# Kernel optimization log

Hardware: AMD Instinct MI355X
Metric: run time of the kernel (lower is better)

## Reference

```python
import jax, jax.numpy as jnp
import numpy as np

NUM_HEADS = 16

def setup_inputs() -> dict:
    key = jax.random.key(0)
    k1, k2, k3 = jax.random.split(key, 3)
    B, N, C = 4, 1024, 1024
    x = jax.random.normal(k1, (B, N, C), dtype=jnp.float32)
    w_qkv = jax.random.normal(k2, (C, 3 * C), dtype=jnp.float32) * (C ** -0.5)
    b_qkv = jnp.zeros((3 * C,), dtype=jnp.float32)
    w_proj = jax.random.normal(k3, (C, C), dtype=jnp.float32) * (C ** -0.5)
    b_proj = jnp.zeros((C,), dtype=jnp.float32)
    return {"x": x, "w_qkv": w_qkv, "b_qkv": b_qkv, "w_proj": w_proj, "b_proj": b_proj}

def reference(x, w_qkv, b_qkv, w_proj, b_proj):
    B, N, C = x.shape
    H = NUM_HEADS
    D = C // H
    scale = D ** -0.5
    # qkv projection: [B,N,3C] -> [3,B,H,N,D]
    qkv = (x @ w_qkv + b_qkv).reshape(B, N, 3, H, D).transpose(2, 0, 3, 1, 4)
    q, k, v = qkv[0], qkv[1], qkv[2]
    q = q * scale
    attn = jnp.einsum('bhnd,bhmd->bhnm', q, k)  # full N x N scores
    attn = jax.nn.softmax(attn, axis=-1)
    out = jnp.einsum('bhnm,bhmd->bhnd', attn, v)  # [B,H,N,D]
    out = out.transpose(0, 2, 1, 3).reshape(B, N, C)
    return out @ w_proj + b_proj
```

## Files before the change

### kernel.cpp

```cpp
#include <hip/hip_runtime.h>

typedef unsigned short u16;
typedef unsigned int u32;
typedef __attribute__((ext_vector_type(8))) short bf16x8;
typedef __attribute__((ext_vector_type(4))) float f32x4;
typedef __attribute__((ext_vector_type(16))) float f32x16;

#define LOG2E 1.4426950408889634f
#define QSCALE (0.125f * LOG2E)

__device__ __forceinline__ u16 f2bf(float f) {
  union { float f; u32 u; } x; x.f = f;
  u32 r = x.u + 0x7fffu + ((x.u >> 16) & 1u);
  return (u16)(r >> 16);
}

__device__ __forceinline__ u32 cvtpk(float a, float b) {
  u32 r;
  asm("v_cvt_pk_bf16_f32 %0, %1, %2" : "=v"(r) : "v"(a), "v"(b));
  return r;
}

__device__ __forceinline__ bf16x8 mkfrag(u32 a, u32 b, u32 c, u32 d) {
  union { u32 w[4]; bf16x8 v; } u;
  u.w[0] = a; u.w[1] = b; u.w[2] = c; u.w[3] = d;
  return u.v;
}

__device__ __forceinline__ void gload_lds16(const void* g, void* l) {
  __builtin_amdgcn_global_load_lds((const __attribute__((address_space(1))) u32*)g,
                                   (__attribute__((address_space(3))) u32*)l, 16, 0, 0);
}

__global__ __launch_bounds__(256) void k_cvt_x(const float* __restrict__ in, u16* __restrict__ out) {
  int i = blockIdx.x * 256 + threadIdx.x;
  const float4* p = (const float4*)in;
  float4 a = p[i * 2], b = p[i * 2 + 1];
  uint4 o;
  o.x = (u32)f2bf(a.x) | ((u32)f2bf(a.y) << 16);
  o.y = (u32)f2bf(a.z) | ((u32)f2bf(a.w) << 16);
  o.z = (u32)f2bf(b.x) | ((u32)f2bf(b.y) << 16);
  o.w = (u32)f2bf(b.z) | ((u32)f2bf(b.w) << 16);
  ((uint4*)out)[i] = o;
}

__global__ __launch_bounds__(256) void k_transpose_cvt(const float* __restrict__ src, u16* __restrict__ dst,
                                                       int R, int Cc) {
  __shared__ float tile[32][33];
  int c0 = blockIdx.x * 32, r0 = blockIdx.y * 32;
  int tx = threadIdx.x, ty = threadIdx.y;
  #pragma unroll
  for (int j = 0; j < 4; ++j)
    tile[ty * 4 + j][tx] = src[(r0 + ty * 4 + j) * Cc + c0 + tx];
  __syncthreads();
  #pragma unroll
  for (int j = 0; j < 4; ++j) {
    int cl = ty * 4 + j;
    dst[(c0 + cl) * R + r0 + tx] = f2bf(tile[tx][cl]);
  }
}

template <int EPI, int NBN>
__global__ __launch_bounds__(256) void k_gemm(const u16* __restrict__ A, const u16* __restrict__ Bt,
                                              const float* __restrict__ bias,
                                              u16* __restrict__ oq, u16* __restrict__ ok,
                                              u16* __restrict__ ovt, float* __restrict__ of) {
  __shared__ u16 lds[24576];
  const int tid = threadIdx.x;
  const int l = tid & 63, w = tid >> 6;
  const int wm = w >> 1, wn = w & 1;
  const int lr = l & 15, lh = l >> 4;
  const int cpx = gridDim.x >> 3;
  const int wg = (blockIdx.x & 7) * cpx + (blockIdx.x >> 3);
  const int bn = wg % NBN, bm = wg / NBN;

  f32x4 acc[4][4] = {};
  const int e = tid * 8;
  const u16* gA = A + (bm * 128 + (e >> 5)) * 1024 + (e & 31);
  const u16* gB = Bt + (bn * 128 + (e >> 5)) * 1024 + (e & 31);

  #define GSTAGE(kk, b)                                              \
    do {                                                             \
      gload_lds16(gA + (kk),         lds + (b) * 8192 + e);          \
      gload_lds16(gA + (kk) + 65536, lds + (b) * 8192 + e + 2048);   \
      gload_lds16(gB + (kk),         lds + (b) * 8192 + 4096 + e);   \
      gload_lds16(gB + (kk) + 65536, lds + (b) * 8192 + 4096 + e + 2048); \
    } while (0)

  GSTAGE(0, 0);
  GSTAGE(32, 1);
  int cur = 0, nxt = 2;

  for (int it = 0; it < 32; ++it) {
    if (it < 31) asm volatile("s_waitcnt vmcnt(4)" ::: "memory");
    else         asm volatile("s_waitcnt vmcnt(0)" ::: "memory");
    __builtin_amdgcn_s_barrier();
    __builtin_amdgcn_sched_barrier(0);

    if (it < 30) GSTAGE((it + 2) * 32, nxt);

    const u16* Asc = lds + cur * 8192;
    const u16* Bsc = lds + cur * 8192 + 4096;
    bf16x8 af[4], bfr[4];
    #pragma unroll
    for (int mi = 0; mi < 4; ++mi)
      af[mi] = *(const bf16x8*)(Asc + (wm * 64 + mi * 16 + lr) * 32 + lh * 8);
    #pragma unroll
    for (int ni = 0; ni < 4; ++ni)
      bfr[ni] = *(const bf16x8*)(Bsc + (wn * 64 + ni * 16 + lr) * 32 + lh * 8);
    #pragma unroll
    for (int mi = 0; mi < 4; ++mi)
      #pragma unroll
      for (int ni = 0; ni < 4; ++ni)
        acc[mi][ni] = __builtin_amdgcn_mfma_f32_16x16x32_bf16(af[mi], bfr[ni], acc[mi][ni], 0, 0, 0);

    cur = (cur == 2) ? 0 : cur + 1;
    nxt = (nxt == 2) ? 0 : nxt + 1;
  }
  #undef GSTAGE

  if (EPI == 0) {
    #pragma unroll
    for (int ni = 0; ni < 4; ++ni) {
      int col = bn * 128 + wn * 64 + ni * 16 + lr;
      float bb = bias[col];
      #pragma unroll
      for (int mi = 0; mi < 4; ++mi) {
        int row = bm * 128 + wm * 64 + mi * 16 + lh * 4;
        #pragma unroll
        for (int r = 0; r < 4; ++r)
          of[(row + r) * (NBN * 128) + col] = acc[mi][ni][r] + bb;
      }
    }
  } else {
    const int s = bn >> 3;
    __syncthreads();
    if (s < 2) {
      u16* dst = (s == 0) ? oq : ok;
      const float sc = (s == 0) ? QSCALE : 1.0f;
      #pragma unroll
      for (int ni = 0; ni < 4; ++ni) {
        int cl = wn * 64 + ni * 16 + lr;
        float bb = bias[bn * 128 + cl];
        #pragma unroll
        for (int mi = 0; mi < 4; ++mi) {
          int rl = wm * 64 + mi * 16 + lh * 4;
          #pragma unroll
          for (int r = 0; r < 4; ++r)
            lds[(rl + r) * 136 + cl] = f2bf((acc[mi][ni][r] + bb) * sc);
        }
      }
      __syncthreads();
      const int row = tid >> 1, half = tid & 1;
      const int h0 = ((bn * 128) & 1023) >> 6;
      const int b = (bm * 128) >> 10, n0 = (bm * 128) & 1023;
      const u16* srow = lds + row * 136 + half * 64;
      u16* drow = dst + ((u32)((b * 16 + h0 + half) * 1024) + n0 + row) * 64;
      #pragma unroll
      for (int j = 0; j < 8; ++j)
        *(uint4*)(drow + j * 8) = *(const uint4*)(srow + j * 8);
    } else {
      #pragma unroll
      for (int ni = 0; ni < 4; ++ni) {
        int cl = wn * 64 + ni * 16 + lr;
        float bb = bias[bn * 128 + cl];
        #pragma unroll
        for (int mi = 0; mi < 4; ++mi) {
          int rl = wm * 64 + mi * 16 + lh * 4;
          u32 p0 = (u32)f2bf(acc[mi][ni][0] + bb) | ((u32)f2bf(acc[mi][ni][1] + bb) << 16);
          u32 p1 = (u32)f2bf(acc[mi][ni][2] + bb) | ((u32)f2bf(acc[mi][ni][3] + bb) << 16);
          uint2 pk; pk.x = p0; pk.y = p1;
          *(uint2*)(lds + cl * 136 + rl) = pk;
        }
      }
      __syncthreads();
      int cl = tid >> 1, half = tid & 1;
      int c = bn * 128 + cl, cc = c & 1023, h = cc >> 6, d = cc & 63;
      int b = (bm * 128) >> 10, n0 = (bm * 128) & 1023;
      const u16* srow = lds + cl * 136 + half * 64;
      u16* drow = ovt + ((b * 16 + h) * 64 + d) * 1024 + n0 + half * 64;
      #pragma unroll
      for (int j = 0; j < 8; ++j)
        *(uint4*)(drow + j * 8) = *(const uint4*)(srow + j * 8);
    }
  }
}

__global__ __launch_bounds__(256) void k_attn(const u16* __restrict__ q, const u16* __restrict__ k,
                                              const u16* __restrict__ vt, u16* __restrict__ ao) {
  __shared__ u16 Ks[2][4096], Vs[2][4096];
  const int tid = threadIdx.x, l = tid & 63, w = tid >> 6;
  const int lq = l & 31;
  const int hi = l >> 5;
  const int i = blockIdx.x;
  const int bh = (i & 7) * 8 + ((i >> 3) & 7);
  const int qb = i >> 6;

  const int qrow = qb * 128 + w * 32 + lq;
  const u16* qg = q + bh * 65536 + qrow * 64;
  bf16x8 qf[4];
  #pragma unroll
  for (int ks = 0; ks < 4; ++ks)
    qf[ks] = *(const bf16x8*)(qg + ks * 16 + hi * 8);

  float mr = -1e30f, lsum = 0.f;
  f32x16 o0 = {}, o1 = {};

  const u16* kg = k + bh * 65536;
  const u16* vg = vt + bh * 65536;

  const int ch0 = tid, ch1 = 256 + tid;
  const int r0_ = ch0 >> 3, s0_ = (ch0 & 7) ^ (r0_ & 7);
  const int r1_ = ch1 >> 3, s1_ = (ch1 & 7) ^ (r1_ & 7);

  #define STAGE(t, buf)                                                        \
    do {                                                                       \
      gload_lds16(kg + (t) * 4096 + r0_ * 64 + s0_ * 8, Ks[buf] + ch0 * 8);    \
      gload_lds16(vg + r0_ * 1024 + (t) * 64 + s0_ * 8, Vs[buf] + ch0 * 8);    \
      gload_lds16(kg + (t) * 4096 + r1_ * 64 + s1_ * 8, Ks[buf] + ch1 * 8);    \
      gload_lds16(vg + r1_ * 1024 + (t) * 64 + s1_ * 8, Vs[buf] + ch1 * 8);    \
    } while (0)

  STAGE(0, 0);

  const int swz = (lq & 7) << 4;

  for (int t = 0; t < 16; ++t) {
    const int cur = t & 1;
    if (t < 15) {
      STAGE(t + 1, cur ^ 1);
      asm volatile("s_waitcnt vmcnt(4)" ::: "memory");
    } else {
      asm volatile("s_waitcnt vmcnt(0)" ::: "memory");
    }
    __builtin_amdgcn_s_barrier();
    __builtin_amdgcn_sched_barrier(0);

    f32x16 sA = {}, sB = {};
    __builtin_amdgcn_s_setprio(1);
    #pragma unroll
    for (int ks = 0; ks < 4; ++ks) {
      bf16x8 kf0 = *(const bf16x8*)((const char*)Ks[cur] + (((lq) * 128 + ks * 32 + hi * 16) ^ swz));
      bf16x8 kf1 = *(const bf16x8*)((const char*)Ks[cur] + (((32 + lq) * 128 + ks * 32 + hi * 16) ^ swz));
      sA = __builtin_amdgcn_mfma_f32_32x32x16_bf16(kf0, qf[ks], sA, 0, 0, 0);
      sB = __builtin_amdgcn_mfma_f32_32x32x16_bf16(kf1, qf[ks], sB, 0, 0, 0);
    }
    __builtin_amdgcn_s_setprio(0);

    float pmax = sA[0];
    #pragma unroll
    for (int r = 1; r < 16; ++r) pmax = fmaxf(pmax, sA[r]);
    #pragma unroll
    for (int r = 0; r < 16; ++r) pmax = fmaxf(pmax, sB[r]);
    pmax = fmaxf(pmax, __shfl_xor(pmax, 32));

    if (!__all(pmax - mr <= 8.0f)) {
      float nm = fmaxf(mr, pmax);
      float al = __builtin_amdgcn_exp2f(mr - nm);
      mr = nm;
      lsum *= al;
      #pragma unroll
      for (int r = 0; r < 16; ++r) {
        int row = (r & 3) + 8 * (r >> 2) + 4 * hi;
        float f = __shfl(al, row, 64);
        o0[r] *= f; o1[r] *= f;
      }
    }

    float ls = 0.f;
    #pragma unroll
    for (int r = 0; r < 16; ++r) { float e = __builtin_amdgcn_exp2f(sA[r] - mr); sA[r] = e; ls += e; }
    #pragma unroll
    for (int r = 0; r < 16; ++r) { float e = __builtin_amdgcn_exp2f(sB[r] - mr); sB[r] = e; ls += e; }
    lsum += ls;

    u32 wa[8], wb[8];
    #pragma unroll
    for (int j = 0; j < 8; ++j) {
      wa[j] = cvtpk(sA[2 * j], sA[2 * j + 1]);
      wb[j] = cvtpk(sB[2 * j], sB[2 * j + 1]);
    }
    u32 xa0 = __shfl_xor((int)wa[0], 32), xa1 = __shfl_xor((int)wa[1], 32);
    u32 xa2 = __shfl_xor((int)wa[2], 32), xa3 = __shfl_xor((int)wa[3], 32);
    u32 xa4 = __shfl_xor((int)wa[4], 32), xa5 = __shfl_xor((int)wa[5], 32);
    u32 xa6 = __shfl_xor((int)wa[6], 32), xa7 = __shfl_xor((int)wa[7], 32);
    u32 xb0 = __shfl_xor((int)wb[0], 32), xb1 = __shfl_xor((int)wb[1], 32);
    u32 xb2 = __shfl_xor((int)wb[2], 32), xb3 = __shfl_xor((int)wb[3], 32);
    u32 xb4 = __shfl_xor((int)wb[4], 32), xb5 = __shfl_xor((int)wb[5], 32);
    u32 xb6 = __shfl_xor((int)wb[6], 32), xb7 = __shfl_xor((int)wb[7], 32);
    bf16x8 pa0 = mkfrag(hi ? xa2 : wa[0], hi ? xa3 : wa[1], hi ? wa[2] : xa0, hi ? wa[3] : xa1);
    bf16x8 pa1 = mkfrag(hi ? xa6 : wa[4], hi ? xa7 : wa[5], hi ? wa[6] : xa4, hi ? wa[7] : xa5);
    bf16x8 pa2 = mkfrag(hi ? xb2 : wb[0], hi ? xb3 : wb[1], hi ? wb[2] : xb0, hi ? wb[3] : xb1);
    bf16x8 pa3 = mkfrag(hi ? xb6 : wb[4], hi ? xb7 : wb[5], hi ? wb[6] : xb4, hi ? wb[7] : xb5);

    __builtin_amdgcn_s_setprio(1);
    #pragma unroll
    for (int ks = 0; ks < 4; ++ks) {
      bf16x8 pf = (ks == 0) ? pa0 : (ks == 1) ? pa1 : (ks == 2) ? pa2 : pa3;
      bf16x8 vf0 = *(const bf16x8*)((const char*)Vs[cur] + (((lq) * 128 + ks * 32 + hi * 16) ^ swz));
      bf16x8 vf1 = *(const bf16x8*)((const char*)Vs[cur] + (((32 + lq) * 128 + ks * 32 + hi * 16) ^ swz));
      o0 = __builtin_amdgcn_mfma_f32_32x32x16_bf16(pf, vf0, o0, 0, 0, 0);
      o1 = __builtin_amdgcn_mfma_f32_32x32x16_bf16(pf, vf1, o1, 0, 0, 0);
    }
    __builtin_amdgcn_s_setprio(0);

    __builtin_amdgcn_s_barrier();
  }
  #undef STAGE

  lsum += __shfl_xor(lsum, 32);
  const int b = bh >> 4, h = bh & 15;
  u16* aob = ao + (u32)(b * 1024 + qb * 128 + w * 32) * 1024 + h * 64;
  #pragma unroll
  for (int r = 0; r < 16; ++r) {
    int row = (r & 3) + 8 * (r >> 2) + 4 * hi;
    float inv = 1.0f / __shfl(lsum, row, 64);
    aob[row * 1024 + lq]      = f2bf(o0[r] * inv);
    aob[row * 1024 + 32 + lq] = f2bf(o1[r] * inv);
  }
}

extern "C" void kernel_launch(void* const* d_in, const int* in_sizes, int n_in,
                              void* d_out, int out_size, void* d_ws, size_t ws_size,
                              hipStream_t stream) {
  const float* x      = (const float*)d_in[0];
  const float* w_qkv  = (const float*)d_in[1];
  const float* b_qkv  = (const float*)d_in[2];
  const float* w_proj = (const float*)d_in[3];
  const float* b_proj = (const float*)d_in[4];
  float* out = (float*)d_out;
  char* ws = (char*)d_ws;

  u16* X16   = (u16*)ws;
  u16* Wqkv  = (u16*)(ws + 8388608);
  u16* Wproj = (u16*)(ws + 14680064);
  u16* Q     = (u16*)(ws + 16777216);
  u16* K     = (u16*)(ws + 25165824);
  u16* VT    = (u16*)(ws + 33554432);
  u16* AO    = X16;

  k_cvt_x<<<dim3(2048), dim3(256), 0, stream>>>(x, X16);
  k_transpose_cvt<<<dim3(96, 32), dim3(32, 8), 0, stream>>>(w_qkv, Wqkv, 1024, 3072);
  k_transpose_cvt<<<dim3(32, 32), dim3(32, 8), 0, stream>>>(w_proj, Wproj, 1024, 1024);
  k_gemm<1, 24><<<dim3(768), dim3(256), 0, stream>>>(X16, Wqkv, b_qkv, Q, K, VT, (float*)0);
  k_attn<<<dim3(512), dim3(256), 0, stream>>>(Q, K, VT, AO);
  k_gemm<0, 8><<<dim3(256), dim3(256), 0, stream>>>(AO, Wproj, b_proj, (u16*)0, (u16*)0, (u16*)0, out);
}
```

Baseline: 103.8 us.

## Use 8 warps per GEMM block and XOR-swizzle LDS tiles

The GEMM kernel goes from 4 to 8 wavefronts per 128x128 tile. Each wave now computes a 64x32 sub-tile with half the accumulators, and each thread issues one global-to-LDS load per operand per stage instead of two. The LDS layout gains an XOR swizzle on the 16-byte column group to cut bank conflicts on fragment reads. The epilogue stores are respread over 512 threads. The change trades lower register pressure and more latency hiding for more LDS fragment reads per MFMA, since A fragments are now loaded by 4 waves instead of 2.

```diff
diff --git a/kernel.cpp b/kernel.cpp
--- a/kernel.cpp
+++ b/kernel.cpp
@@ -61,30 +61,31 @@
 }
 
 template <int EPI, int NBN>
-__global__ __launch_bounds__(256) void k_gemm(const u16* __restrict__ A, const u16* __restrict__ Bt,
+__global__ __launch_bounds__(512) void k_gemm(const u16* __restrict__ A, const u16* __restrict__ Bt,
                                               const float* __restrict__ bias,
                                               u16* __restrict__ oq, u16* __restrict__ ok,
                                               u16* __restrict__ ovt, float* __restrict__ of) {
   __shared__ u16 lds[24576];
   const int tid = threadIdx.x;
   const int l = tid & 63, w = tid >> 6;
-  const int wm = w >> 1, wn = w & 1;
+  const int wm = w >> 2, wn = w & 3;
   const int lr = l & 15, lh = l >> 4;
   const int cpx = gridDim.x >> 3;
   const int wg = (blockIdx.x & 7) * cpx + (blockIdx.x >> 3);
   const int bn = wg % NBN, bm = wg / NBN;
 
-  f32x4 acc[4][4] = {};
+  f32x4 acc[4][2] = {};
   const int e = tid * 8;
-  const u16* gA = A + (bm * 128 + (e >> 5)) * 1024 + (e & 31);
-  const u16* gB = Bt + (bn * 128 + (e >> 5)) * 1024 + (e & 31);
+  const int srow = e >> 5;
+  const int sgr  = (e >> 3) & 3;
+  const int scol = (sgr ^ ((srow >> 1) & 3)) * 8;
+  const u16* gA = A + (bm * 128 + srow) * 1024 + scol;
+  const u16* gB = Bt + (bn * 128 + srow) * 1024 + scol;
 
   #define GSTAGE(kk, b)                                              \
     do {                                                             \
-      gload_lds16(gA + (kk),         lds + (b) * 8192 + e);          \
-      gload_lds16(gA + (kk) + 65536, lds + (b) * 8192 + e + 2048);   \
-      gload_lds16(gB + (kk),         lds + (b) * 8192 + 4096 + e);   \
-      gload_lds16(gB + (kk) + 65536, lds + (b) * 8192 + 4096 + e + 2048); \
+      gload_lds16(gA + (kk), lds + (b) * 8192 + e);                  \
+      gload_lds16(gB + (kk), lds + (b) * 8192 + 4096 + e);           \
     } while (0)
 
   GSTAGE(0, 0);
@@ -92,7 +93,7 @@
   int cur = 0, nxt = 2;
 
   for (int it = 0; it < 32; ++it) {
-    if (it < 31) asm volatile("s_waitcnt vmcnt(4)" ::: "memory");
+    if (it < 31) asm volatile("s_waitcnt vmcnt(2)" ::: "memory");
     else         asm volatile("s_waitcnt vmcnt(0)" ::: "memory");
     __builtin_amdgcn_s_barrier();
     __builtin_amdgcn_sched_barrier(0);
@@ -100,18 +101,21 @@
     if (it < 30) GSTAGE((it + 2) * 32, nxt);
 
     const u16* Asc = lds + cur * 8192;
-    const u16* Bsc = lds + cur * 8192 + 4096;
-    bf16x8 af[4], bfr[4];
+    bf16x8 af[4], bfr[2];
+    #pragma unroll
+    for (int mi = 0; mi < 4; ++mi) {
+      int r = wm * 64 + mi * 16 + lr;
+      af[mi] = *(const bf16x8*)(Asc + r * 32 + ((lh ^ ((r >> 1) & 3)) * 8));
+    }
+    #pragma unroll
+    for (int ni = 0; ni < 2; ++ni) {
+      int r = wn * 32 + ni * 16 + lr;
+      bfr[ni] = *(const bf16x8*)(Asc + 4096 + r * 32 + ((lh ^ ((r >> 1) & 3)) * 8));
+    }
     #pragma unroll
     for (int mi = 0; mi < 4; ++mi)
-      af[mi] = *(const bf16x8*)(Asc + (wm * 64 + mi * 16 + lr) * 32 + lh * 8);
-    #pragma unroll
-    for (int ni = 0; ni < 4; ++ni)
-      bfr[ni] = *(const bf16x8*)(Bsc + (wn * 64 + ni * 16 + lr) * 32 + lh * 8);
-    #pragma unroll
-    for (int mi = 0; mi < 4; ++mi)
-      #pragma unroll
-      for (int ni = 0; ni < 4; ++ni)
+      #pragma unroll
+      for (int ni = 0; ni < 2; ++ni)
         acc[mi][ni] = __builtin_amdgcn_mfma_f32_16x16x32_bf16(af[mi], bfr[ni], acc[mi][ni], 0, 0, 0);
 
     cur = (cur == 2) ? 0 : cur + 1;
@@ -121,8 +125,8 @@
 
   if (EPI == 0) {
     #pragma unroll
-    for (int ni = 0; ni < 4; ++ni) {
-      int col = bn * 128 + wn * 64 + ni * 16 + lr;
+    for (int ni = 0; ni < 2; ++ni) {
+      int col = bn * 128 + wn * 32 + ni * 16 + lr;
       float bb = bias[col];
       #pragma unroll
       for (int mi = 0; mi < 4; ++mi) {
@@ -139,8 +143,8 @@
       u16* dst = (s == 0) ? oq : ok;
       const float sc = (s == 0) ? QSCALE : 1.0f;
       #pragma unroll
-      for (int ni = 0; ni < 4; ++ni) {
-        int cl = wn * 64 + ni * 16 + lr;
+      for (int ni = 0; ni < 2; ++ni) {
+        int cl = wn * 32 + ni * 16 + lr;
         float bb = bias[bn * 128 + cl];
         #pragma unroll
         for (int mi = 0; mi < 4; ++mi) {
@@ -151,18 +155,18 @@
         }
       }
       __syncthreads();
-      const int row = tid >> 1, half = tid & 1;
+      const int row = tid >> 2, q4 = tid & 3;
       const int h0 = ((bn * 128) & 1023) >> 6;
       const int b = (bm * 128) >> 10, n0 = (bm * 128) & 1023;
-      const u16* srow = lds + row * 136 + half * 64;
-      u16* drow = dst + ((u32)((b * 16 + h0 + half) * 1024) + n0 + row) * 64;
-      #pragma unroll
-      for (int j = 0; j < 8; ++j)
-        *(uint4*)(drow + j * 8) = *(const uint4*)(srow + j * 8);
+      const u16* srow2 = lds + row * 136 + q4 * 32;
+      u16* drow = dst + ((u32)((b * 16 + h0 + (q4 >> 1)) * 1024) + n0 + row) * 64 + (q4 & 1) * 32;
+      #pragma unroll
+      for (int j = 0; j < 4; ++j)
+        *(uint4*)(drow + j * 8) = *(const uint4*)(srow2 + j * 8);
     } else {
       #pragma unroll
-      for (int ni = 0; ni < 4; ++ni) {
-        int cl = wn * 64 + ni * 16 + lr;
+      for (int ni = 0; ni < 2; ++ni) {
+        int cl = wn * 32 + ni * 16 + lr;
         float bb = bias[bn * 128 + cl];
         #pragma unroll
         for (int mi = 0; mi < 4; ++mi) {
@@ -174,14 +178,14 @@
         }
       }
       __syncthreads();
-      int cl = tid >> 1, half = tid & 1;
-      int c = bn * 128 + cl, cc = c & 1023, h = cc >> 6, d = cc & 63;
-      int b = (bm * 128) >> 10, n0 = (bm * 128) & 1023;
-      const u16* srow = lds + cl * 136 + half * 64;
-      u16* drow = ovt + ((b * 16 + h) * 64 + d) * 1024 + n0 + half * 64;
-      #pragma unroll
-      for (int j = 0; j < 8; ++j)
-        *(uint4*)(drow + j * 8) = *(const uint4*)(srow + j * 8);
+      const int cl = tid >> 2, q4 = tid & 3;
+      const int c = bn * 128 + cl, cc = c & 1023, h = cc >> 6, d = cc & 63;
+      const int b = (bm * 128) >> 10, n0 = (bm * 128) & 1023;
+      const u16* srow2 = lds + cl * 136 + q4 * 32;
+      u16* drow = ovt + ((b * 16 + h) * 64 + d) * 1024 + n0 + q4 * 32;
+      #pragma unroll
+      for (int j = 0; j < 4; ++j)
+        *(uint4*)(drow + j * 8) = *(const uint4*)(srow2 + j * 8);
     }
   }
 }
@@ -342,7 +346,7 @@
   k_cvt_x<<<dim3(2048), dim3(256), 0, stream>>>(x, X16);
   k_transpose_cvt<<<dim3(96, 32), dim3(32, 8), 0, stream>>>(w_qkv, Wqkv, 1024, 3072);
   k_transpose_cvt<<<dim3(32, 32), dim3(32, 8), 0, stream>>>(w_proj, Wproj, 1024, 1024);
-  k_gemm<1, 24><<<dim3(768), dim3(256), 0, stream>>>(X16, Wqkv, b_qkv, Q, K, VT, (float*)0);
+  k_gemm<1, 24><<<dim3(768), dim3(512), 0, stream>>>(X16, Wqkv, b_qkv, Q, K, VT, (float*)0);
   k_attn<<<dim3(512), dim3(256), 0, stream>>>(Q, K, VT, AO);
-  k_gemm<0, 8><<<dim3(256), dim3(256), 0, stream>>>(AO, Wproj, b_proj, (u16*)0, (u16*)0, (u16*)0, out);
-}
+  k_gemm<0, 8><<<dim3(256), dim3(512), 0, stream>>>(AO, Wproj, b_proj, (u16*)0, (u16*)0, (u16*)0, out);
+}
```

Measured after the change: 99.87 us. 3.8% less time.
